# Kernel tuning notes

Measured on AMD Instinct MI355X. Metric: run time of the kernel, lower is better.

The kernel has to match this reference:

```python
import jax, jax.numpy as jnp
import numpy as np

F_NODE = 256   # node_feat_size
H      = 256   # hidden_size (must equal F_NODE due to expand using feat_size)
M      = 128   # max_child_num
T      = 4     # edge_type_num
ITERS  = 2     # num_iterations
NSEM   = 57    # Tree.num_sem


def setup_inputs() -> dict:
    key = jax.random.key(0)
    ks = jax.random.split(key, 12)

    def lin(k, fan_in, shape):
        return jax.random.normal(k, shape, jnp.float32) / np.sqrt(fan_in).astype(np.float32)

    return dict(
        parent_feature=jax.random.normal(ks[0], (1, F_NODE), jnp.float32),
        gt_children_code=jax.random.normal(ks[1], (1, 16), jnp.float32),
        gt_num_code=jax.random.normal(ks[2], (1, 10), jnp.float32),
        W_parent=lin(ks[3], F_NODE + 26, (F_NODE + 26, H * M)),
        b_parent=jnp.zeros((H * M,), jnp.float32),
        W_exists=lin(ks[4], H, (H, 1)),
        b_exists=jnp.zeros((1,), jnp.float32),
        W_sem=lin(ks[5], H, (H, NSEM)),
        b_sem=jnp.zeros((NSEM,), jnp.float32),
        W_el=lin(ks[6], 2 * H, (2 * H, H)),
        b_el=jnp.zeros((H,), jnp.float32),
        W_ee=lin(ks[7], H, (T, H)),          # stacked per-type [H,1] heads
        b_ee=jnp.zeros((T,), jnp.float32),
        W_ne=lin(ks[8], 3 * H + T, (ITERS, 3 * H + T, H)),
        b_ne=jnp.zeros((ITERS, H), jnp.float32),
        W_child=lin(ks[9], (ITERS + 1) * H, ((ITERS + 1) * H, H)),
        b_child=jnp.zeros((H,), jnp.float32),
        W_child2=lin(ks[10], H, (H, F_NODE)),
        b_child2=jnp.zeros((F_NODE,), jnp.float32),
    )


def reference(parent_feature, gt_children_code, gt_num_code,
              W_parent, b_parent, W_exists, b_exists, W_sem, b_sem,
              W_el, b_el, W_ee, b_ee, W_ne, b_ne,
              W_child, b_child, W_child2, b_child2):
    B = parent_feature.shape[0]  # == 1 (message passing uses batch index 0 only)

    pf = jnp.concatenate([parent_feature, gt_children_code, gt_num_code], axis=1)
    child_feats = jax.nn.relu(pf @ W_parent + b_parent).reshape(B, M, H)

    child_exists_logits = child_feats @ W_exists + b_exists           # [B,M,1]

    # pairwise edge latents [B,M,M,H]
    pair = jnp.concatenate([
        jnp.broadcast_to(child_feats[:, :, None, :], (B, M, M, H)),
        jnp.broadcast_to(child_feats[:, None, :, :], (B, M, M, H)),
    ], axis=3)
    edge_latents = jax.nn.relu(pair @ W_el + b_el)                    # [B,M,M,H]
    edge_exists_logits = jnp.einsum('bijh,th->bijt', edge_latents, W_ee) + b_ee  # [B,M,M,T]

    # --- masked full candidate edge set (replaces data-dependent torch.nonzero) ---
    ii, jj, tt = jnp.meshgrid(jnp.arange(M), jnp.arange(M), jnp.arange(T), indexing='ij')
    i = ii.reshape(-1)   # [E] source nodes
    j = jj.reshape(-1)
    t = tt.reshape(-1)

    logit_e = edge_exists_logits[0].reshape(-1)                        # [E], same (i,j,t) order
    exists0 = child_exists_logits[0, :, 0] > 0                         # [M]
    mask = (logit_e > 0) & exists0[i] & exists0[j]                     # [E]
    maskf = mask.astype(child_feats.dtype)[:, None]

    edge_feats_mp = edge_latents[0][i, j]                              # [E,H]
    edge_type_logit = jax.nn.one_hot(t, T, dtype=logit_e.dtype) * logit_e[:, None]  # [E,T]
    ef = jnp.concatenate([edge_feats_mp, edge_type_logit], axis=1)     # [E,H+T]

    cf0 = child_feats[0]                                               # [M,H]
    iter_feats = [cf0]
    for it in range(ITERS):
        x = jnp.concatenate([cf0[i], cf0[j], ef], axis=1)              # [E,3H+T]
        msg = jax.nn.relu(x @ W_ne[it] + b_ne[it]) * maskf             # masked msgs are 0
        # scatter_max with zero-initialized out (relu msgs >= 0, matches torch_scatter out=zeros)
        cf0 = jnp.zeros((M, H), msg.dtype).at[i].max(msg)
        iter_feats.append(cf0)

    all_feats = jnp.concatenate(iter_feats, axis=1)                    # [M,(ITERS+1)H]
    h = jax.nn.relu(all_feats @ W_child + b_child)                     # [M,H]
    child_sem_logits = (h @ W_sem + b_sem)[None]                       # [1,M,NSEM]
    child_out = jax.nn.relu(h @ W_child2 + b_child2)[None]             # [1,M,F_NODE]
    return (child_out, child_sem_logits, child_exists_logits, edge_exists_logits)
```

## Files before the change

kernel.cpp:

```cpp
#include <hip/hip_runtime.h>
#include <hip/hip_bf16.h>
#include <stdint.h>


typedef unsigned short ushort_t;
using f32x4 = __attribute__((ext_vector_type(4))) float;
using s16x8 = __attribute__((ext_vector_type(8))) short;

__device__ __forceinline__ ushort_t f2bf(float x) {
  __hip_bfloat16 h = __float2bfloat16(x);
  return *reinterpret_cast<ushort_t*>(&h);
}

__global__ __launch_bounds__(256) void k1_parent(
    const float* __restrict__ p0, const float* __restrict__ p1, const float* __restrict__ p2,
    const float* __restrict__ W, const float* __restrict__ b, float* __restrict__ cf) {
  __shared__ float pfs[282];
  __shared__ f32x4 red[320];
  int tid = threadIdx.x;
  pfs[tid] = p0[tid];
  if (tid < 16) pfs[256 + tid] = p1[tid];
  if (tid < 10) pfs[272 + tid] = p2[tid];
  __syncthreads();
  int c = tid & 7, s = tid >> 3;
  int colg = blockIdx.x * 8 + c;
  const f32x4* W4 = (const f32x4*)W;
  int k0 = (s * 282) >> 5, k1e = ((s + 1) * 282) >> 5;
  f32x4 acc = {0.f, 0.f, 0.f, 0.f};
  #pragma unroll 4
  for (int k = k0; k < k1e; ++k)
    acc += pfs[k] * W4[(size_t)k * 8192 + colg];
  red[s * 8 + c] = acc;
  __syncthreads();
  if (tid < 64) {
    int col = tid & 7, part = tid >> 3;
    f32x4 v = red[(part * 4 + 0) * 8 + col] + red[(part * 4 + 1) * 8 + col]
            + red[(part * 4 + 2) * 8 + col] + red[(part * 4 + 3) * 8 + col];
    red[256 + part * 8 + col] = v;
  }
  __syncthreads();
  if (tid < 8) {
    f32x4 v = red[256 + tid];
    #pragma unroll
    for (int q = 1; q < 8; ++q) v += red[256 + q * 8 + tid];
    v += ((const f32x4*)b)[blockIdx.x * 8 + tid];
    #pragma unroll
    for (int q = 0; q < 4; ++q) v[q] = fmaxf(v[q], 0.f);
    ((f32x4*)cf)[blockIdx.x * 8 + tid] = v;
  }
}

__global__ __launch_bounds__(1024) void ks1(
    const float* __restrict__ cf, const float* __restrict__ Wel,
    const float* __restrict__ Wne, const float* __restrict__ bne,
    const float* __restrict__ Wex, const float* __restrict__ bex,
    float* __restrict__ A, float* __restrict__ B, float* __restrict__ P,
    float* __restrict__ Q, float* __restrict__ ex0, float* __restrict__ exout,
    ushort_t* __restrict__ W3T) {
  __shared__ float c[256];
  __shared__ float redA[1024], redB[1024], redP[1024], redQ[1024];
  __shared__ float wsum[4];
  int tid = threadIdx.x;
  int r = blockIdx.x >> 1, half = blockIdx.x & 1;
  if (tid < 256) c[tid] = cf[r * 256 + tid];
  __syncthreads();
  int cc = tid & 127, s = tid >> 7;
  int col = half * 128 + cc;
  int k0 = s * 32;
  const float* WelB = Wel + 256 * 256;
  float aA = 0.f, aB = 0.f, aP = 0.f, aQ = 0.f;
  #pragma unroll 4
  for (int kk = 0; kk < 32; ++kk) {
    int k = k0 + kk;
    float cv = c[k];
    aA += cv * Wel[k * 256 + col];
    aB += cv * WelB[k * 256 + col];
    aP += cv * Wne[k * 256 + col];
    aQ += cv * Wne[(256 + k) * 256 + col];
  }
  redA[tid] = aA; redB[tid] = aB; redP[tid] = aP; redQ[tid] = aQ;
  float v = (half == 0 && tid < 256) ? c[tid] * Wex[tid] : 0.f;
  #pragma unroll
  for (int off = 32; off; off >>= 1) v += __shfl_xor(v, off);
  if (half == 0 && tid < 256 && (tid & 63) == 0) wsum[tid >> 6] = v;
  __syncthreads();
  if (tid < 128) {
    int cl = half * 128 + tid;
    float a = 0.f, bb = 0.f, pv = bne[cl], qv = 0.f;
    #pragma unroll
    for (int q = 0; q < 8; ++q) {
      a  += redA[q * 128 + tid];
      bb += redB[q * 128 + tid];
      pv += redP[q * 128 + tid];
      qv += redQ[q * 128 + tid];
    }
    A[r * 256 + cl] = a;
    B[r * 256 + cl] = bb;
    P[r * 256 + cl] = pv;
    Q[r * 256 + cl] = qv;
  }
  if (half == 0 && tid == 0) {
    float lg = wsum[0] + wsum[1] + wsum[2] + wsum[3] + bex[0];
    exout[r] = lg;
    ex0[r] = lg > 0.f ? 1.f : 0.f;
  }
  if (tid < 512) {
    int idx = blockIdx.x * 512 + tid;
    int it = idx >> 16, n = (idx >> 8) & 255, k = idx & 255;
    W3T[it * 65536 + n * 256 + (k ^ ((n & 7) << 3))] =
        f2bf(Wne[(size_t)(it * 772 + 512 + k) * 256 + n]);
  }
}

__global__ __launch_bounds__(256) void k3_edge(
    const float* __restrict__ A, const float* __restrict__ B, const float* __restrict__ bel,
    const float* __restrict__ Wee, const float* __restrict__ bee,
    ushort_t* __restrict__ ELbf, float* __restrict__ elog) {
  __shared__ float w4s[4][4][4];
  int tid = threadIdx.x, lane = tid & 63, wid = tid >> 6;
  int p0 = blockIdx.x * 4;
  int i = p0 >> 7;
  float a = A[i * 256 + tid] + bel[tid];
  float we0 = Wee[tid], we1 = Wee[256 + tid], we2 = Wee[512 + tid], we3 = Wee[768 + tid];
  #pragma unroll
  for (int jj = 0; jj < 4; ++jj) {
    int pr = p0 + jj;
    int j = pr & 127;
    float el = fmaxf(a + B[j * 256 + tid], 0.f);
    ELbf[(size_t)pr * 256 + (tid ^ ((pr & 7) << 3))] = f2bf(el);
    float t0 = el * we0, t1 = el * we1, t2 = el * we2, t3 = el * we3;
    #pragma unroll
    for (int off = 32; off; off >>= 1) {
      t0 += __shfl_xor(t0, off);
      t1 += __shfl_xor(t1, off);
      t2 += __shfl_xor(t2, off);
      t3 += __shfl_xor(t3, off);
    }
    if (lane == 0) { w4s[jj][wid][0] = t0; w4s[jj][wid][1] = t1;
                     w4s[jj][wid][2] = t2; w4s[jj][wid][3] = t3; }
  }
  __syncthreads();
  if (tid < 16) {
    int jj = tid >> 2, t = tid & 3;
    float v = w4s[jj][0][t] + w4s[jj][1][t] + w4s[jj][2][t] + w4s[jj][3][t] + bee[t];
    elog[(p0 + jj) * 4 + t] = v;
  }
}

__global__ __launch_bounds__(256) void kf(
    const ushort_t* __restrict__ ELbf, const ushort_t* __restrict__ W3T_it,
    const float* __restrict__ Wne_it, const float* __restrict__ P,
    const float* __restrict__ Q, const float* __restrict__ ex0,
    const float* __restrict__ elog, float* __restrict__ cfn) {
  __shared__ __align__(16) ushort_t lA[128 * 64];
  __shared__ __align__(16) ushort_t lB[128 * 64];
  __shared__ float sl[512];
  __shared__ float se[128];
  __shared__ float red[256];
  int tid = threadIdx.x;
  int i = blockIdx.x >> 1, nh = blockIdx.x & 1;
  if (ex0[i] == 0.f) {
    if (tid < 128) cfn[i * 256 + nh * 128 + tid] = 0.f;
    return;
  }
  sl[tid] = elog[i * 512 + tid];
  sl[256 + tid] = elog[i * 512 + 256 + tid];
  if (tid < 128) se[tid] = ex0[tid];
  int lane = tid & 63, wid = tid >> 6;
  int wr = wid >> 1, wc = wid & 1;
  f32x4 acc[4][4] = {};
  for (int ks = 0; ks < 256; ks += 64) {
    __syncthreads();
    #pragma unroll
    for (int rr = 0; rr < 4; ++rr) {
      int c = rr * 4 + wid;
      int row = c * 8 + (lane >> 3);
      int co = (lane & 7) * 8;
      const ushort_t* sa = ELbf + (size_t)(i * 128 + row) * 256 + ks + co;
      const ushort_t* sb = W3T_it + (size_t)(nh * 128 + row) * 256 + ks + co;
      __builtin_amdgcn_global_load_lds((const __attribute__((address_space(1))) void*)sa,
                                       (__attribute__((address_space(3))) void*)(lA + c * 512), 16, 0, 0);
      __builtin_amdgcn_global_load_lds((const __attribute__((address_space(1))) void*)sb,
                                       (__attribute__((address_space(3))) void*)(lB + c * 512), 16, 0, 0);
    }
    __syncthreads();
    #pragma unroll
    for (int kk = 0; kk < 2; ++kk) {
      s16x8 af[4], bfr[4];
      #pragma unroll
      for (int mt = 0; mt < 4; ++mt) {
        int row = wr * 64 + mt * 16 + (lane & 15);
        int kl = (kk * 32 + (lane >> 4) * 8) ^ ((row & 7) << 3);
        af[mt] = *reinterpret_cast<const s16x8*>(&lA[row * 64 + kl]);
      }
      #pragma unroll
      for (int nt = 0; nt < 4; ++nt) {
        int row = wc * 64 + nt * 16 + (lane & 15);
        int kl = (kk * 32 + (lane >> 4) * 8) ^ ((row & 7) << 3);
        bfr[nt] = *reinterpret_cast<const s16x8*>(&lB[row * 64 + kl]);
      }
      #pragma unroll
      for (int mt = 0; mt < 4; ++mt)
        #pragma unroll
        for (int nt = 0; nt < 4; ++nt)
          acc[mt][nt] = __builtin_amdgcn_mfma_f32_16x16x32_bf16(af[mt], bfr[nt], acc[mt][nt], 0, 0, 0);
    }
  }
  __syncthreads();
  const float NEG = -3.0e38f;
  #pragma unroll
  for (int nt = 0; nt < 4; ++nt) {
    int col_l = wc * 64 + nt * 16 + (lane & 15);
    int col = nh * 128 + col_l;
    float w40 = Wne_it[768 * 256 + col];
    float w41 = Wne_it[769 * 256 + col];
    float w42 = Wne_it[770 * 256 + col];
    float w43 = Wne_it[771 * 256 + col];
    float mx = NEG;
    #pragma unroll
    for (int mt = 0; mt < 4; ++mt)
      #pragma unroll
      for (int r = 0; r < 4; ++r) {
        int j = wr * 64 + mt * 16 + (lane >> 4) * 4 + r;
        float base = acc[mt][nt][r] + Q[j * 256 + col];
        float sej = se[j];
        float l0 = sl[j * 4 + 0], l1 = sl[j * 4 + 1];
        float l2 = sl[j * 4 + 2], l3 = sl[j * 4 + 3];
        if (sej > 0.f) {
          if (l0 > 0.f) mx = fmaxf(mx, base + l0 * w40);
          if (l1 > 0.f) mx = fmaxf(mx, base + l1 * w41);
          if (l2 > 0.f) mx = fmaxf(mx, base + l2 * w42);
          if (l3 > 0.f) mx = fmaxf(mx, base + l3 * w43);
        }
      }
    mx = fmaxf(mx, __shfl_xor(mx, 16));
    mx = fmaxf(mx, __shfl_xor(mx, 32));
    if (lane < 16) red[wr * 128 + col_l] = mx;
  }
  __syncthreads();
  if (tid < 128) {
    float m = fmaxf(red[tid], red[128 + tid]);
    float v = P[i * 256 + nh * 128 + tid] + m;
    cfn[i * 256 + nh * 128 + tid] = fmaxf(v, 0.f);
  }
}

__global__ __launch_bounds__(1024) void kp1(
    const float* __restrict__ cf, const float* __restrict__ Wne_it,
    const float* __restrict__ bne_it, float* __restrict__ P, float* __restrict__ Q) {
  __shared__ float c[256];
  __shared__ float redP[1024], redQ[1024];
  int tid = threadIdx.x;
  int r = blockIdx.x >> 1, half = blockIdx.x & 1;
  if (tid < 256) c[tid] = cf[r * 256 + tid];
  __syncthreads();
  int cc = tid & 127, s = tid >> 7;
  int col = half * 128 + cc;
  int k0 = s * 32;
  float aP = 0.f, aQ = 0.f;
  #pragma unroll 4
  for (int kk = 0; kk < 32; ++kk) {
    int k = k0 + kk;
    float cv = c[k];
    aP += cv * Wne_it[k * 256 + col];
    aQ += cv * Wne_it[(256 + k) * 256 + col];
  }
  redP[tid] = aP; redQ[tid] = aQ;
  __syncthreads();
  if (tid < 128) {
    int cl = half * 128 + tid;
    float pv = bne_it[cl], qv = 0.f;
    #pragma unroll
    for (int q = 0; q < 8; ++q) { pv += redP[q * 128 + tid]; qv += redQ[q * 128 + tid]; }
    P[r * 256 + cl] = pv;
    Q[r * 256 + cl] = qv;
  }
}

__global__ __launch_bounds__(1024) void k6_final(
    const float* __restrict__ cf0, const float* __restrict__ cf1, const float* __restrict__ cf2,
    const float* __restrict__ Wc, const float* __restrict__ bc,
    const float* __restrict__ Wsem, const float* __restrict__ bsem,
    const float* __restrict__ W2, const float* __restrict__ b2,
    float* __restrict__ out) {
  __shared__ float af[768];
  __shared__ float red[1024];
  __shared__ float hb[256];
  __shared__ float redS[4 * 57];
  int tid = threadIdx.x, m = blockIdx.x;
  if (tid < 768) {
    af[tid] = tid < 256 ? cf0[m * 256 + tid]
            : tid < 512 ? cf1[m * 256 + tid - 256]
                        : cf2[m * 256 + tid - 512];
  }
  __syncthreads();
  int cc = tid & 255, s = tid >> 8;
  {
    float acc = 0.f;
    #pragma unroll 4
    for (int kk = 0; kk < 192; ++kk) {
      int k = s * 192 + kk;
      acc += af[k] * Wc[k * 256 + cc];
    }
    red[tid] = acc;
  }
  __syncthreads();
  if (tid < 256) {
    float v = bc[tid] + red[tid] + red[256 + tid] + red[512 + tid] + red[768 + tid];
    hb[tid] = fmaxf(v, 0.f);
  }
  __syncthreads();
  {
    float acc = 0.f;
    #pragma unroll 4
    for (int kk = 0; kk < 64; ++kk) {
      int k = s * 64 + kk;
      acc += hb[k] * W2[k * 256 + cc];
    }
    red[tid] = acc;
    if (cc < 57) {
      float accs = 0.f;
      #pragma unroll 4
      for (int kk = 0; kk < 64; ++kk) {
        int k = s * 64 + kk;
        accs += hb[k] * Wsem[k * 57 + cc];
      }
      redS[s * 57 + cc] = accs;
    }
  }
  __syncthreads();
  if (tid < 256) {
    float v = b2[tid] + red[tid] + red[256 + tid] + red[512 + tid] + red[768 + tid];
    out[m * 256 + tid] = fmaxf(v, 0.f);
  }
  if (tid < 57) {
    float v = bsem[tid] + redS[tid] + redS[57 + tid] + redS[114 + tid] + redS[171 + tid];
    out[32768 + m * 57 + tid] = v;
  }
}

extern "C" void kernel_launch(void* const* d_in, const int* in_sizes, int n_in,
                              void* d_out, int out_size, void* d_ws, size_t ws_size,
                              hipStream_t stream) {
  const float* p0  = (const float*)d_in[0];
  const float* p1  = (const float*)d_in[1];
  const float* p2  = (const float*)d_in[2];
  const float* Wp  = (const float*)d_in[3];
  const float* bp  = (const float*)d_in[4];
  const float* Wex = (const float*)d_in[5];
  const float* bex = (const float*)d_in[6];
  const float* Wsm = (const float*)d_in[7];
  const float* bsm = (const float*)d_in[8];
  const float* Wel = (const float*)d_in[9];
  const float* bel = (const float*)d_in[10];
  const float* Wee = (const float*)d_in[11];
  const float* bee = (const float*)d_in[12];
  const float* Wne = (const float*)d_in[13];
  const float* bne = (const float*)d_in[14];
  const float* Wc  = (const float*)d_in[15];
  const float* bc  = (const float*)d_in[16];
  const float* W2  = (const float*)d_in[17];
  const float* b2  = (const float*)d_in[18];
  float* out = (float*)d_out;

  char* ws = (char*)d_ws;
  float*    cf0  = (float*)(ws + 0);
  float*    cf1  = (float*)(ws + 131072);
  float*    cf2  = (float*)(ws + 262144);
  float*    Ab   = (float*)(ws + 393216);
  float*    Bb   = (float*)(ws + 524288);
  float*    Pb   = (float*)(ws + 655360);
  float*    Qb   = (float*)(ws + 786432);
  float*    ex0  = (float*)(ws + 917504);
  ushort_t* W3T  = (ushort_t*)(ws + 1048576);
  ushort_t* ELbf = (ushort_t*)(ws + 2097152);

  float* out_ex = out + 40064;
  float* out_el = out + 40192;

  k1_parent<<<1024, 256, 0, stream>>>(p0, p1, p2, Wp, bp, cf0);
  ks1<<<256, 1024, 0, stream>>>(cf0, Wel, Wne, bne, Wex, bex,
                                Ab, Bb, Pb, Qb, ex0, out_ex, W3T);
  k3_edge<<<4096, 256, 0, stream>>>(Ab, Bb, bel, Wee, bee, ELbf, out_el);
  kf<<<256, 256, 0, stream>>>(ELbf, W3T, Wne, Pb, Qb, ex0, out_el, cf1);
  kp1<<<256, 1024, 0, stream>>>(cf1, Wne + 772 * 256, bne + 256, Pb, Qb);
  kf<<<256, 256, 0, stream>>>(ELbf, W3T + 65536, Wne + 772 * 256, Pb, Qb, ex0, out_el, cf2);
  k6_final<<<128, 1024, 0, stream>>>(cf0, cf1, cf2, Wc, bc, Wsm, bsm, W2, b2, out);
}
```

Before: 216.4 us.

## Fuse message-passing iterations with P/Q projection and final MLP per row

The message kernel now handles a whole output row (all 256 columns) per 512-thread block instead of splitting columns across two blocks. The next-iteration P/Q projection is folded into the first kernel's epilogue, and the final child MLP (W_child, W_child2, W_sem) into the second kernel's epilogue. This drops two launches and the intermediate global round trips, and uses separate P/Q buffers so the second iteration does not overwrite inputs still being read. The cost is half as many blocks (128 instead of 256), so fewer CUs are busy during the MFMA phase, and the serial per-row epilogue gets longer.

```diff
diff --git a/kernel.cpp b/kernel.cpp
--- a/kernel.cpp
+++ b/kernel.cpp
@@ -147,195 +147,176 @@
   }
 }
 
-__global__ __launch_bounds__(256) void kf(
+template<int MODE>
+__global__ __launch_bounds__(512) void kf_row(
     const ushort_t* __restrict__ ELbf, const ushort_t* __restrict__ W3T_it,
     const float* __restrict__ Wne_it, const float* __restrict__ P,
     const float* __restrict__ Q, const float* __restrict__ ex0,
-    const float* __restrict__ elog, float* __restrict__ cfn) {
+    const float* __restrict__ elog, float* __restrict__ cfn,
+    float* __restrict__ Pn, float* __restrict__ Qn,
+    const float* __restrict__ bne_n, const float* __restrict__ WneN,
+    const float* __restrict__ cf0, const float* __restrict__ cf1,
+    const float* __restrict__ Wc, const float* __restrict__ bc,
+    const float* __restrict__ W2, const float* __restrict__ b2,
+    const float* __restrict__ Wsem, const float* __restrict__ bsem,
+    float* __restrict__ out) {
   __shared__ __align__(16) ushort_t lA[128 * 64];
-  __shared__ __align__(16) ushort_t lB[128 * 64];
+  __shared__ __align__(16) ushort_t lB[256 * 64];
   __shared__ float sl[512];
   __shared__ float se[128];
-  __shared__ float red[256];
+  __shared__ float redm[512];
+  __shared__ float cfrow[256];
+  __shared__ float hrow[256];
   int tid = threadIdx.x;
-  int i = blockIdx.x >> 1, nh = blockIdx.x & 1;
-  if (ex0[i] == 0.f) {
-    if (tid < 128) cfn[i * 256 + nh * 128 + tid] = 0.f;
-    return;
-  }
-  sl[tid] = elog[i * 512 + tid];
-  sl[256 + tid] = elog[i * 512 + 256 + tid];
-  if (tid < 128) se[tid] = ex0[tid];
+  int i = blockIdx.x;
   int lane = tid & 63, wid = tid >> 6;
-  int wr = wid >> 1, wc = wid & 1;
-  f32x4 acc[4][4] = {};
-  for (int ks = 0; ks < 256; ks += 64) {
-    __syncthreads();
-    #pragma unroll
-    for (int rr = 0; rr < 4; ++rr) {
-      int c = rr * 4 + wid;
-      int row = c * 8 + (lane >> 3);
-      int co = (lane & 7) * 8;
-      const ushort_t* sa = ELbf + (size_t)(i * 128 + row) * 256 + ks + co;
-      const ushort_t* sb = W3T_it + (size_t)(nh * 128 + row) * 256 + ks + co;
-      __builtin_amdgcn_global_load_lds((const __attribute__((address_space(1))) void*)sa,
-                                       (__attribute__((address_space(3))) void*)(lA + c * 512), 16, 0, 0);
-      __builtin_amdgcn_global_load_lds((const __attribute__((address_space(1))) void*)sb,
-                                       (__attribute__((address_space(3))) void*)(lB + c * 512), 16, 0, 0);
-    }
-    __syncthreads();
-    #pragma unroll
-    for (int kk = 0; kk < 2; ++kk) {
-      s16x8 af[4], bfr[4];
+  int wr = wid >> 2, wc = wid & 3;
+  bool alive = ex0[i] != 0.f;
+  if (alive) {
+    sl[tid] = elog[i * 512 + tid];
+    if (tid < 128) se[tid] = ex0[tid];
+    f32x4 acc[4][4] = {};
+    for (int ks = 0; ks < 256; ks += 64) {
+      __syncthreads();
       #pragma unroll
-      for (int mt = 0; mt < 4; ++mt) {
-        int row = wr * 64 + mt * 16 + (lane & 15);
-        int kl = (kk * 32 + (lane >> 4) * 8) ^ ((row & 7) << 3);
-        af[mt] = *reinterpret_cast<const s16x8*>(&lA[row * 64 + kl]);
+      for (int rr = 0; rr < 2; ++rr) {
+        int c = rr * 8 + wid;
+        int row = c * 8 + (lane >> 3);
+        int co = (lane & 7) * 8;
+        const ushort_t* sa = ELbf + (size_t)(i * 128 + row) * 256 + ks + co;
+        __builtin_amdgcn_global_load_lds((const __attribute__((address_space(1))) void*)sa,
+                                         (__attribute__((address_space(3))) void*)(lA + c * 512), 16, 0, 0);
       }
       #pragma unroll
-      for (int nt = 0; nt < 4; ++nt) {
-        int row = wc * 64 + nt * 16 + (lane & 15);
-        int kl = (kk * 32 + (lane >> 4) * 8) ^ ((row & 7) << 3);
-        bfr[nt] = *reinterpret_cast<const s16x8*>(&lB[row * 64 + kl]);
+      for (int rr = 0; rr < 4; ++rr) {
+        int c = rr * 8 + wid;
+        int row = c * 8 + (lane >> 3);
+        int co = (lane & 7) * 8;
+        const ushort_t* sb = W3T_it + (size_t)row * 256 + ks + co;
+        __builtin_amdgcn_global_load_lds((const __attribute__((address_space(1))) void*)sb,
+                                         (__attribute__((address_space(3))) void*)(lB + c * 512), 16, 0, 0);
       }
+      __syncthreads();
+      #pragma unroll
+      for (int kk = 0; kk < 2; ++kk) {
+        s16x8 af[4], bfr[4];
+        #pragma unroll
+        for (int mt = 0; mt < 4; ++mt) {
+          int row = wr * 64 + mt * 16 + (lane & 15);
+          int kl = (kk * 32 + (lane >> 4) * 8) ^ ((row & 7) << 3);
+          af[mt] = *reinterpret_cast<const s16x8*>(&lA[row * 64 + kl]);
+        }
+        #pragma unroll
+        for (int nt = 0; nt < 4; ++nt) {
+          int n = wc * 64 + nt * 16 + (lane & 15);
+          int kl = (kk * 32 + (lane >> 4) * 8) ^ ((n & 7) << 3);
+          bfr[nt] = *reinterpret_cast<const s16x8*>(&lB[n * 64 + kl]);
+        }
+        #pragma unroll
+        for (int mt = 0; mt < 4; ++mt)
+          #pragma unroll
+          for (int nt = 0; nt < 4; ++nt)
+            acc[mt][nt] = __builtin_amdgcn_mfma_f32_16x16x32_bf16(af[mt], bfr[nt], acc[mt][nt], 0, 0, 0);
+      }
+    }
+    __syncthreads();
+    const float NEG = -3.0e38f;
+    #pragma unroll
+    for (int nt = 0; nt < 4; ++nt) {
+      int col = wc * 64 + nt * 16 + (lane & 15);
+      float w40 = Wne_it[768 * 256 + col];
+      float w41 = Wne_it[769 * 256 + col];
+      float w42 = Wne_it[770 * 256 + col];
+      float w43 = Wne_it[771 * 256 + col];
+      float mx = NEG;
       #pragma unroll
       for (int mt = 0; mt < 4; ++mt)
         #pragma unroll
-        for (int nt = 0; nt < 4; ++nt)
-          acc[mt][nt] = __builtin_amdgcn_mfma_f32_16x16x32_bf16(af[mt], bfr[nt], acc[mt][nt], 0, 0, 0);
-    }
-  }
-  __syncthreads();
-  const float NEG = -3.0e38f;
-  #pragma unroll
-  for (int nt = 0; nt < 4; ++nt) {
-    int col_l = wc * 64 + nt * 16 + (lane & 15);
-    int col = nh * 128 + col_l;
-    float w40 = Wne_it[768 * 256 + col];
-    float w41 = Wne_it[769 * 256 + col];
-    float w42 = Wne_it[770 * 256 + col];
-    float w43 = Wne_it[771 * 256 + col];
-    float mx = NEG;
-    #pragma unroll
-    for (int mt = 0; mt < 4; ++mt)
-      #pragma unroll
-      for (int r = 0; r < 4; ++r) {
-        int j = wr * 64 + mt * 16 + (lane >> 4) * 4 + r;
-        float base = acc[mt][nt][r] + Q[j * 256 + col];
-        float sej = se[j];
-        float l0 = sl[j * 4 + 0], l1 = sl[j * 4 + 1];
-        float l2 = sl[j * 4 + 2], l3 = sl[j * 4 + 3];
-        if (sej > 0.f) {
-          if (l0 > 0.f) mx = fmaxf(mx, base + l0 * w40);
-          if (l1 > 0.f) mx = fmaxf(mx, base + l1 * w41);
-          if (l2 > 0.f) mx = fmaxf(mx, base + l2 * w42);
-          if (l3 > 0.f) mx = fmaxf(mx, base + l3 * w43);
+        for (int r = 0; r < 4; ++r) {
+          int j = wr * 64 + mt * 16 + (lane >> 4) * 4 + r;
+          float base = acc[mt][nt][r] + Q[j * 256 + col];
+          float sej = se[j];
+          float l0 = sl[j * 4 + 0], l1 = sl[j * 4 + 1];
+          float l2 = sl[j * 4 + 2], l3 = sl[j * 4 + 3];
+          if (sej > 0.f) {
+            if (l0 > 0.f) mx = fmaxf(mx, base + l0 * w40);
+            if (l1 > 0.f) mx = fmaxf(mx, base + l1 * w41);
+            if (l2 > 0.f) mx = fmaxf(mx, base + l2 * w42);
+            if (l3 > 0.f) mx = fmaxf(mx, base + l3 * w43);
+          }
         }
+      mx = fmaxf(mx, __shfl_xor(mx, 16));
+      mx = fmaxf(mx, __shfl_xor(mx, 32));
+      if (lane < 16) redm[wr * 256 + col] = mx;
+    }
+    __syncthreads();
+    if (tid < 256) {
+      float m = fmaxf(redm[tid], redm[256 + tid]);
+      float v = P[i * 256 + tid] + m;
+      cfrow[tid] = fmaxf(v, 0.f);
+    }
+  } else {
+    if (tid < 256) cfrow[tid] = 0.f;
+  }
+  __syncthreads();
+  if (tid < 256) cfn[i * 256 + tid] = cfrow[tid];
+
+  int cc = tid & 255, s = tid >> 8;
+  if (MODE == 0) {
+    float aP = 0.f, aQ = 0.f;
+    #pragma unroll 4
+    for (int kk = 0; kk < 128; ++kk) {
+      int k = s * 128 + kk;
+      float cv = cfrow[k];
+      aP += cv * WneN[k * 256 + cc];
+      aQ += cv * WneN[(256 + k) * 256 + cc];
+    }
+    redm[s * 256 + cc] = aP;
+    sl[s * 256 + cc] = aQ;
+    __syncthreads();
+    if (tid < 256) {
+      Pn[i * 256 + tid] = bne_n[tid] + redm[tid] + redm[256 + tid];
+      Qn[i * 256 + tid] = sl[tid] + sl[256 + tid];
+    }
+  } else {
+    float* af = (float*)lA;
+    if (tid < 256) {
+      af[tid] = cf0[i * 256 + tid];
+      af[256 + tid] = cf1[i * 256 + tid];
+      af[512 + tid] = cfrow[tid];
+    }
+    __syncthreads();
+    float acc2 = 0.f;
+    #pragma unroll 4
+    for (int kk = 0; kk < 384; ++kk) {
+      int k = s * 384 + kk;
+      acc2 += af[k] * Wc[k * 256 + cc];
+    }
+    redm[s * 256 + cc] = acc2;
+    __syncthreads();
+    if (tid < 256) hrow[tid] = fmaxf(bc[tid] + redm[tid] + redm[256 + tid], 0.f);
+    __syncthreads();
+    float acc3 = 0.f;
+    #pragma unroll 4
+    for (int kk = 0; kk < 128; ++kk) {
+      int k = s * 128 + kk;
+      acc3 += hrow[k] * W2[k * 256 + cc];
+    }
+    redm[s * 256 + cc] = acc3;
+    float accS = 0.f;
+    if (cc < 57) {
+      #pragma unroll 4
+      for (int kk = 0; kk < 128; ++kk) {
+        int k = s * 128 + kk;
+        accS += hrow[k] * Wsem[k * 57 + cc];
       }
-    mx = fmaxf(mx, __shfl_xor(mx, 16));
-    mx = fmaxf(mx, __shfl_xor(mx, 32));
-    if (lane < 16) red[wr * 128 + col_l] = mx;
-  }
-  __syncthreads();
-  if (tid < 128) {
-    float m = fmaxf(red[tid], red[128 + tid]);
-    float v = P[i * 256 + nh * 128 + tid] + m;
-    cfn[i * 256 + nh * 128 + tid] = fmaxf(v, 0.f);
-  }
-}
-
-__global__ __launch_bounds__(1024) void kp1(
-    const float* __restrict__ cf, const float* __restrict__ Wne_it,
-    const float* __restrict__ bne_it, float* __restrict__ P, float* __restrict__ Q) {
-  __shared__ float c[256];
-  __shared__ float redP[1024], redQ[1024];
-  int tid = threadIdx.x;
-  int r = blockIdx.x >> 1, half = blockIdx.x & 1;
-  if (tid < 256) c[tid] = cf[r * 256 + tid];
-  __syncthreads();
-  int cc = tid & 127, s = tid >> 7;
-  int col = half * 128 + cc;
-  int k0 = s * 32;
-  float aP = 0.f, aQ = 0.f;
-  #pragma unroll 4
-  for (int kk = 0; kk < 32; ++kk) {
-    int k = k0 + kk;
-    float cv = c[k];
-    aP += cv * Wne_it[k * 256 + col];
-    aQ += cv * Wne_it[(256 + k) * 256 + col];
-  }
-  redP[tid] = aP; redQ[tid] = aQ;
-  __syncthreads();
-  if (tid < 128) {
-    int cl = half * 128 + tid;
-    float pv = bne_it[cl], qv = 0.f;
-    #pragma unroll
-    for (int q = 0; q < 8; ++q) { pv += redP[q * 128 + tid]; qv += redQ[q * 128 + tid]; }
-    P[r * 256 + cl] = pv;
-    Q[r * 256 + cl] = qv;
-  }
-}
-
-__global__ __launch_bounds__(1024) void k6_final(
-    const float* __restrict__ cf0, const float* __restrict__ cf1, const float* __restrict__ cf2,
-    const float* __restrict__ Wc, const float* __restrict__ bc,
-    const float* __restrict__ Wsem, const float* __restrict__ bsem,
-    const float* __restrict__ W2, const float* __restrict__ b2,
-    float* __restrict__ out) {
-  __shared__ float af[768];
-  __shared__ float red[1024];
-  __shared__ float hb[256];
-  __shared__ float redS[4 * 57];
-  int tid = threadIdx.x, m = blockIdx.x;
-  if (tid < 768) {
-    af[tid] = tid < 256 ? cf0[m * 256 + tid]
-            : tid < 512 ? cf1[m * 256 + tid - 256]
-                        : cf2[m * 256 + tid - 512];
-  }
-  __syncthreads();
-  int cc = tid & 255, s = tid >> 8;
-  {
-    float acc = 0.f;
-    #pragma unroll 4
-    for (int kk = 0; kk < 192; ++kk) {
-      int k = s * 192 + kk;
-      acc += af[k] * Wc[k * 256 + cc];
-    }
-    red[tid] = acc;
-  }
-  __syncthreads();
-  if (tid < 256) {
-    float v = bc[tid] + red[tid] + red[256 + tid] + red[512 + tid] + red[768 + tid];
-    hb[tid] = fmaxf(v, 0.f);
-  }
-  __syncthreads();
-  {
-    float acc = 0.f;
-    #pragma unroll 4
-    for (int kk = 0; kk < 64; ++kk) {
-      int k = s * 64 + kk;
-      acc += hb[k] * W2[k * 256 + cc];
-    }
-    red[tid] = acc;
-    if (cc < 57) {
-      float accs = 0.f;
-      #pragma unroll 4
-      for (int kk = 0; kk < 64; ++kk) {
-        int k = s * 64 + kk;
-        accs += hb[k] * Wsem[k * 57 + cc];
-      }
-      redS[s * 57 + cc] = accs;
-    }
-  }
-  __syncthreads();
-  if (tid < 256) {
-    float v = b2[tid] + red[tid] + red[256 + tid] + red[512 + tid] + red[768 + tid];
-    out[m * 256 + tid] = fmaxf(v, 0.f);
-  }
-  if (tid < 57) {
-    float v = bsem[tid] + redS[tid] + redS[57 + tid] + redS[114 + tid] + redS[171 + tid];
-    out[32768 + m * 57 + tid] = v;
+      sl[s * 64 + cc] = accS;
+    }
+    __syncthreads();
+    if (tid < 256)
+      out[i * 256 + tid] = fmaxf(b2[tid] + redm[tid] + redm[256 + tid], 0.f);
+    if (tid < 57)
+      out[32768 + i * 57 + tid] = bsem[tid] + sl[tid] + sl[64 + tid];
   }
 }
 
@@ -371,19 +352,26 @@
   float*    Bb   = (float*)(ws + 524288);
   float*    Pb   = (float*)(ws + 655360);
   float*    Qb   = (float*)(ws + 786432);
-  float*    ex0  = (float*)(ws + 917504);
-  ushort_t* W3T  = (ushort_t*)(ws + 1048576);
+  float*    Pb2  = (float*)(ws + 917504);
+  float*    Qb2  = (float*)(ws + 1048576);
+  float*    ex0  = (float*)(ws + 1179648);
+  ushort_t* W3T  = (ushort_t*)(ws + 1310720);
   ushort_t* ELbf = (ushort_t*)(ws + 2097152);
 
   float* out_ex = out + 40064;
   float* out_el = out + 40192;
+
+  const float* Wne1 = Wne + 772 * 256;
 
   k1_parent<<<1024, 256, 0, stream>>>(p0, p1, p2, Wp, bp, cf0);
   ks1<<<256, 1024, 0, stream>>>(cf0, Wel, Wne, bne, Wex, bex,
                                 Ab, Bb, Pb, Qb, ex0, out_ex, W3T);
   k3_edge<<<4096, 256, 0, stream>>>(Ab, Bb, bel, Wee, bee, ELbf, out_el);
-  kf<<<256, 256, 0, stream>>>(ELbf, W3T, Wne, Pb, Qb, ex0, out_el, cf1);
-  kp1<<<256, 1024, 0, stream>>>(cf1, Wne + 772 * 256, bne + 256, Pb, Qb);
-  kf<<<256, 256, 0, stream>>>(ELbf, W3T + 65536, Wne + 772 * 256, Pb, Qb, ex0, out_el, cf2);
-  k6_final<<<128, 1024, 0, stream>>>(cf0, cf1, cf2, Wc, bc, Wsm, bsm, W2, b2, out);
-}
+  kf_row<0><<<128, 512, 0, stream>>>(ELbf, W3T, Wne, Pb, Qb, ex0, out_el, cf1,
+                                     Pb2, Qb2, bne + 256, Wne1,
+                                     nullptr, nullptr, nullptr, nullptr,
+                                     nullptr, nullptr, nullptr, nullptr, nullptr);
+  kf_row<1><<<128, 512, 0, stream>>>(ELbf, W3T + 65536, Wne1, Pb2, Qb2, ex0, out_el, cf2,
+                                     nullptr, nullptr, nullptr, nullptr,
+                                     cf0, cf1, Wc, bc, W2, b2, Wsm, bsm, out);
+}
```

After: 221.6 us. 1.02x slower.

## Stage full K in LDS for kf with 512 threads; split k6_final columns

Applied to the files above, without the earlier changes.

The message-passing kernel kf now loads the entire 128x256 bf16 A and B tiles into LDS in one pass, using 128KB of shared memory. This replaces four K-steps that each had two barriers. It runs 8 waves in a 2x4 layout, and prefetches Q, P and the type-weight values into registers before the MFMA loop. k6_final splits each row's output columns across two blocks, so it launches 256 blocks to add parallelism; the first matmul is recomputed in both blocks. Separate P/Q buffers are used for the second iteration. The large LDS footprint limits kf to one block per CU.

```diff
diff --git a/kernel.cpp b/kernel.cpp
--- a/kernel.cpp
+++ b/kernel.cpp
@@ -147,13 +147,13 @@
   }
 }
 
-__global__ __launch_bounds__(256) void kf(
+__global__ __launch_bounds__(512) void kf(
     const ushort_t* __restrict__ ELbf, const ushort_t* __restrict__ W3T_it,
     const float* __restrict__ Wne_it, const float* __restrict__ P,
     const float* __restrict__ Q, const float* __restrict__ ex0,
     const float* __restrict__ elog, float* __restrict__ cfn) {
-  __shared__ __align__(16) ushort_t lA[128 * 64];
-  __shared__ __align__(16) ushort_t lB[128 * 64];
+  __shared__ __align__(16) ushort_t lA[128 * 256];
+  __shared__ __align__(16) ushort_t lB[128 * 256];
   __shared__ float sl[512];
   __shared__ float se[128];
   __shared__ float red[256];
@@ -163,85 +163,86 @@
     if (tid < 128) cfn[i * 256 + nh * 128 + tid] = 0.f;
     return;
   }
+  int lane = tid & 63, wid = tid >> 6;
+  int wr = wid >> 2, wc = wid & 3;
   sl[tid] = elog[i * 512 + tid];
-  sl[256 + tid] = elog[i * 512 + 256 + tid];
   if (tid < 128) se[tid] = ex0[tid];
-  int lane = tid & 63, wid = tid >> 6;
-  int wr = wid >> 1, wc = wid & 1;
-  f32x4 acc[4][4] = {};
-  for (int ks = 0; ks < 256; ks += 64) {
-    __syncthreads();
-    #pragma unroll
-    for (int rr = 0; rr < 4; ++rr) {
-      int c = rr * 4 + wid;
-      int row = c * 8 + (lane >> 3);
-      int co = (lane & 7) * 8;
-      const ushort_t* sa = ELbf + (size_t)(i * 128 + row) * 256 + ks + co;
-      const ushort_t* sb = W3T_it + (size_t)(nh * 128 + row) * 256 + ks + co;
-      __builtin_amdgcn_global_load_lds((const __attribute__((address_space(1))) void*)sa,
-                                       (__attribute__((address_space(3))) void*)(lA + c * 512), 16, 0, 0);
-      __builtin_amdgcn_global_load_lds((const __attribute__((address_space(1))) void*)sb,
-                                       (__attribute__((address_space(3))) void*)(lB + c * 512), 16, 0, 0);
-    }
-    __syncthreads();
-    #pragma unroll
-    for (int kk = 0; kk < 2; ++kk) {
-      s16x8 af[4], bfr[4];
-      #pragma unroll
-      for (int mt = 0; mt < 4; ++mt) {
-        int row = wr * 64 + mt * 16 + (lane & 15);
-        int kl = (kk * 32 + (lane >> 4) * 8) ^ ((row & 7) << 3);
-        af[mt] = *reinterpret_cast<const s16x8*>(&lA[row * 64 + kl]);
-      }
-      #pragma unroll
-      for (int nt = 0; nt < 4; ++nt) {
-        int row = wc * 64 + nt * 16 + (lane & 15);
-        int kl = (kk * 32 + (lane >> 4) * 8) ^ ((row & 7) << 3);
-        bfr[nt] = *reinterpret_cast<const s16x8*>(&lB[row * 64 + kl]);
-      }
-      #pragma unroll
-      for (int mt = 0; mt < 4; ++mt)
-        #pragma unroll
-        for (int nt = 0; nt < 4; ++nt)
-          acc[mt][nt] = __builtin_amdgcn_mfma_f32_16x16x32_bf16(af[mt], bfr[nt], acc[mt][nt], 0, 0, 0);
-    }
-  }
-  __syncthreads();
-  const float NEG = -3.0e38f;
-  #pragma unroll
-  for (int nt = 0; nt < 4; ++nt) {
-    int col_l = wc * 64 + nt * 16 + (lane & 15);
-    int col = nh * 128 + col_l;
-    float w40 = Wne_it[768 * 256 + col];
-    float w41 = Wne_it[769 * 256 + col];
-    float w42 = Wne_it[770 * 256 + col];
-    float w43 = Wne_it[771 * 256 + col];
-    float mx = NEG;
+  float pv = (tid < 128) ? P[i * 256 + nh * 128 + tid] : 0.f;
+  float qv[2][16];
+  float w4v[2][4];
+  #pragma unroll
+  for (int nt = 0; nt < 2; ++nt) {
+    int col = nh * 128 + wc * 32 + nt * 16 + (lane & 15);
+    #pragma unroll
+    for (int t = 0; t < 4; ++t) w4v[nt][t] = Wne_it[(768 + t) * 256 + col];
     #pragma unroll
     for (int mt = 0; mt < 4; ++mt)
       #pragma unroll
       for (int r = 0; r < 4; ++r) {
         int j = wr * 64 + mt * 16 + (lane >> 4) * 4 + r;
-        float base = acc[mt][nt][r] + Q[j * 256 + col];
-        float sej = se[j];
-        float l0 = sl[j * 4 + 0], l1 = sl[j * 4 + 1];
-        float l2 = sl[j * 4 + 2], l3 = sl[j * 4 + 3];
-        if (sej > 0.f) {
-          if (l0 > 0.f) mx = fmaxf(mx, base + l0 * w40);
-          if (l1 > 0.f) mx = fmaxf(mx, base + l1 * w41);
-          if (l2 > 0.f) mx = fmaxf(mx, base + l2 * w42);
-          if (l3 > 0.f) mx = fmaxf(mx, base + l3 * w43);
+        qv[nt][mt * 4 + r] = Q[j * 256 + col];
+      }
+  }
+  #pragma unroll
+  for (int rr = 0; rr < 8; ++rr) {
+    int c = rr * 8 + wid;
+    const ushort_t* sa = ELbf + (size_t)(i * 128) * 256 + c * 512 + lane * 8;
+    const ushort_t* sb = W3T_it + (size_t)(nh * 128) * 256 + c * 512 + lane * 8;
+    __builtin_amdgcn_global_load_lds((const __attribute__((address_space(1))) void*)sa,
+                                     (__attribute__((address_space(3))) void*)(lA + c * 512), 16, 0, 0);
+    __builtin_amdgcn_global_load_lds((const __attribute__((address_space(1))) void*)sb,
+                                     (__attribute__((address_space(3))) void*)(lB + c * 512), 16, 0, 0);
+  }
+  __syncthreads();
+  f32x4 acc[4][2] = {};
+  #pragma unroll
+  for (int ks = 0; ks < 8; ++ks) {
+    s16x8 af[4], bfr[2];
+    #pragma unroll
+    for (int mt = 0; mt < 4; ++mt) {
+      int row = wr * 64 + mt * 16 + (lane & 15);
+      int kl = (ks * 32 + (lane >> 4) * 8) ^ ((row & 7) << 3);
+      af[mt] = *reinterpret_cast<const s16x8*>(&lA[row * 256 + kl]);
+    }
+    #pragma unroll
+    for (int nt = 0; nt < 2; ++nt) {
+      int n = wc * 32 + nt * 16 + (lane & 15);
+      int kl = (ks * 32 + (lane >> 4) * 8) ^ ((n & 7) << 3);
+      bfr[nt] = *reinterpret_cast<const s16x8*>(&lB[n * 256 + kl]);
+    }
+    #pragma unroll
+    for (int mt = 0; mt < 4; ++mt)
+      #pragma unroll
+      for (int nt = 0; nt < 2; ++nt)
+        acc[mt][nt] = __builtin_amdgcn_mfma_f32_16x16x32_bf16(af[mt], bfr[nt], acc[mt][nt], 0, 0, 0);
+  }
+  const float NEG = -3.0e38f;
+  #pragma unroll
+  for (int nt = 0; nt < 2; ++nt) {
+    float mx = NEG;
+    #pragma unroll
+    for (int mt = 0; mt < 4; ++mt)
+      #pragma unroll
+      for (int r = 0; r < 4; ++r) {
+        int j = wr * 64 + mt * 16 + (lane >> 4) * 4 + r;
+        float base = acc[mt][nt][r] + qv[nt][mt * 4 + r];
+        if (se[j] > 0.f) {
+          float l0 = sl[j * 4 + 0], l1 = sl[j * 4 + 1];
+          float l2 = sl[j * 4 + 2], l3 = sl[j * 4 + 3];
+          if (l0 > 0.f) mx = fmaxf(mx, base + l0 * w4v[nt][0]);
+          if (l1 > 0.f) mx = fmaxf(mx, base + l1 * w4v[nt][1]);
+          if (l2 > 0.f) mx = fmaxf(mx, base + l2 * w4v[nt][2]);
+          if (l3 > 0.f) mx = fmaxf(mx, base + l3 * w4v[nt][3]);
         }
       }
     mx = fmaxf(mx, __shfl_xor(mx, 16));
     mx = fmaxf(mx, __shfl_xor(mx, 32));
-    if (lane < 16) red[wr * 128 + col_l] = mx;
+    if (lane < 16) red[wr * 128 + wc * 32 + nt * 16 + lane] = mx;
   }
   __syncthreads();
   if (tid < 128) {
     float m = fmaxf(red[tid], red[128 + tid]);
-    float v = P[i * 256 + nh * 128 + tid] + m;
-    cfn[i * 256 + nh * 128 + tid] = fmaxf(v, 0.f);
+    cfn[i * 256 + nh * 128 + tid] = fmaxf(pv + m, 0.f);
   }
 }
 
@@ -285,17 +286,18 @@
     float* __restrict__ out) {
   __shared__ float af[768];
   __shared__ float red[1024];
-  __shared__ float hb[256];
-  __shared__ float redS[4 * 57];
-  int tid = threadIdx.x, m = blockIdx.x;
+  __shared__ float hrow[256];
+  __shared__ float redS[8 * 57];
+  int tid = threadIdx.x;
+  int m = blockIdx.x >> 1, half = blockIdx.x & 1;
   if (tid < 768) {
     af[tid] = tid < 256 ? cf0[m * 256 + tid]
             : tid < 512 ? cf1[m * 256 + tid - 256]
                         : cf2[m * 256 + tid - 512];
   }
   __syncthreads();
-  int cc = tid & 255, s = tid >> 8;
   {
+    int cc = tid & 255, s = tid >> 8;
     float acc = 0.f;
     #pragma unroll 4
     for (int kk = 0; kk < 192; ++kk) {
@@ -307,34 +309,40 @@
   __syncthreads();
   if (tid < 256) {
     float v = bc[tid] + red[tid] + red[256 + tid] + red[512 + tid] + red[768 + tid];
-    hb[tid] = fmaxf(v, 0.f);
-  }
-  __syncthreads();
+    hrow[tid] = fmaxf(v, 0.f);
+  }
+  __syncthreads();
+  int cc = tid & 127, s = tid >> 7;
+  int col = half * 128 + cc;
   {
     float acc = 0.f;
     #pragma unroll 4
-    for (int kk = 0; kk < 64; ++kk) {
-      int k = s * 64 + kk;
-      acc += hb[k] * W2[k * 256 + cc];
+    for (int kk = 0; kk < 32; ++kk) {
+      int k = s * 32 + kk;
+      acc += hrow[k] * W2[k * 256 + col];
     }
     red[tid] = acc;
-    if (cc < 57) {
+    if (half == 0 && cc < 57) {
       float accs = 0.f;
       #pragma unroll 4
-      for (int kk = 0; kk < 64; ++kk) {
-        int k = s * 64 + kk;
-        accs += hb[k] * Wsem[k * 57 + cc];
+      for (int kk = 0; kk < 32; ++kk) {
+        int k = s * 32 + kk;
+        accs += hrow[k] * Wsem[k * 57 + cc];
       }
       redS[s * 57 + cc] = accs;
     }
   }
   __syncthreads();
-  if (tid < 256) {
-    float v = b2[tid] + red[tid] + red[256 + tid] + red[512 + tid] + red[768 + tid];
-    out[m * 256 + tid] = fmaxf(v, 0.f);
-  }
-  if (tid < 57) {
-    float v = bsem[tid] + redS[tid] + redS[57 + tid] + redS[114 + tid] + redS[171 + tid];
+  if (tid < 128) {
+    float v = b2[half * 128 + tid];
+    #pragma unroll
+    for (int q = 0; q < 8; ++q) v += red[q * 128 + tid];
+    out[m * 256 + half * 128 + tid] = fmaxf(v, 0.f);
+  }
+  if (half == 0 && tid < 57) {
+    float v = bsem[tid];
+    #pragma unroll
+    for (int q = 0; q < 8; ++q) v += redS[q * 57 + tid];
     out[32768 + m * 57 + tid] = v;
   }
 }
@@ -371,19 +379,23 @@
   float*    Bb   = (float*)(ws + 524288);
   float*    Pb   = (float*)(ws + 655360);
   float*    Qb   = (float*)(ws + 786432);
-  float*    ex0  = (float*)(ws + 917504);
-  ushort_t* W3T  = (ushort_t*)(ws + 1048576);
+  float*    Pb2  = (float*)(ws + 917504);
+  float*    Qb2  = (float*)(ws + 1048576);
+  float*    ex0  = (float*)(ws + 1179648);
+  ushort_t* W3T  = (ushort_t*)(ws + 1310720);
   ushort_t* ELbf = (ushort_t*)(ws + 2097152);
 
   float* out_ex = out + 40064;
   float* out_el = out + 40192;
+
+  const float* Wne1 = Wne + 772 * 256;
 
   k1_parent<<<1024, 256, 0, stream>>>(p0, p1, p2, Wp, bp, cf0);
   ks1<<<256, 1024, 0, stream>>>(cf0, Wel, Wne, bne, Wex, bex,
                                 Ab, Bb, Pb, Qb, ex0, out_ex, W3T);
   k3_edge<<<4096, 256, 0, stream>>>(Ab, Bb, bel, Wee, bee, ELbf, out_el);
-  kf<<<256, 256, 0, stream>>>(ELbf, W3T, Wne, Pb, Qb, ex0, out_el, cf1);
-  kp1<<<256, 1024, 0, stream>>>(cf1, Wne + 772 * 256, bne + 256, Pb, Qb);
-  kf<<<256, 256, 0, stream>>>(ELbf, W3T + 65536, Wne + 772 * 256, Pb, Qb, ex0, out_el, cf2);
-  k6_final<<<128, 1024, 0, stream>>>(cf0, cf1, cf2, Wc, bc, Wsm, bsm, W2, b2, out);
-}
+  kf<<<256, 512, 0, stream>>>(ELbf, W3T, Wne, Pb, Qb, ex0, out_el, cf1);
+  kp1<<<256, 1024, 0, stream>>>(cf1, Wne1, bne + 256, Pb2, Qb2);
+  kf<<<256, 512, 0, stream>>>(ELbf, W3T + 65536, Wne1, Pb2, Qb2, ex0, out_el, cf2);
+  k6_final<<<256, 1024, 0, stream>>>(cf0, cf1, cf2, Wc, bc, Wsm, bsm, W2, b2, out);
+}
```

Result: faster. 187.8 us (-13.2%).
